# Performance work log

Measured on AMD Instinct MI355X. Metric: run time of the kernel, lower is better.

Reference implementation:

```python
import jax, jax.numpy as jnp
import numpy as np

B, S, D, H = 4, 127, 768, 12
HD = D // H
NS = S + 1
GAMMA = 1.0
NEG_INF = -1e9
EPS = 1e-6


def setup_inputs() -> dict:
    key = jax.random.key(0)
    ks = jax.random.split(key, 12)
    s = 0.02
    return {
        'desc': jax.random.normal(ks[0], (B, S, D), jnp.float32),
        'nve': jax.random.normal(ks[1], (B, NS, D), jnp.float32),
        'mask_M': jax.random.uniform(ks[2], (B, H, S, S), jnp.float32),
        'Wq': jax.random.normal(ks[3], (D, D), jnp.float32) * s,
        'bq': jnp.zeros((D,), jnp.float32),
        'Wk': jax.random.normal(ks[4], (D, D), jnp.float32) * s,
        'bk': jnp.zeros((D,), jnp.float32),
        'Wv': jax.random.normal(ks[5], (D, D), jnp.float32) * s,
        'bv': jnp.zeros((D,), jnp.float32),
        'eW1': jax.random.normal(ks[6], (2 * D, D), jnp.float32) * s,
        'eb1': jnp.zeros((D,), jnp.float32),
        'ln_g': jnp.ones((D,), jnp.float32),
        'ln_b': jnp.zeros((D,), jnp.float32),
        'eW2': jax.random.normal(ks[7], (D, D), jnp.float32) * s,
        'eb2': jnp.zeros((D,), jnp.float32),
        'aW': jax.random.normal(ks[8], (3 * HD,), jnp.float32) * s,
        'ab': jnp.zeros((), jnp.float32),
    }


def _layernorm(x, g, b):
    m = jnp.mean(x, -1, keepdims=True)
    v = jnp.var(x, -1, keepdims=True)
    return (x - m) * jax.lax.rsqrt(v + 1e-5) * g + b


def _adjacency():
    # CLS->Var on, Var->CLS off, Var-Var without self loop
    var_adj = 1.0 - jnp.eye(S, dtype=jnp.float32)
    adj = jnp.zeros((NS, NS), jnp.float32)
    adj = adj.at[1:, 1:].set(var_adj)
    adj = adj.at[0, 1:].set(1.0)
    return adj  # [NS, NS]


def reference(desc, nve, mask_M, Wq, bq, Wk, bk, Wv, bv, eW1, eb1, ln_g, ln_b, eW2, eb2, aW, ab):
    adj = _adjacency()

    def proj(W, bias):
        return (nve @ W + bias).reshape(B, NS, H, HD).transpose(0, 2, 1, 3)  # [B,H,NS,HD]

    q, k, v = proj(Wq, bq), proj(Wk, bk), proj(Wv, bv)

    # edge features: pairwise concat of desc embeddings, CLS edges = [desc, desc]
    node_i = jnp.broadcast_to(desc[:, :, None, :], (B, S, S, D))
    node_j = jnp.broadcast_to(desc[:, None, :, :], (B, S, S, D))
    var_edge = jnp.concatenate([node_i, node_j], -1)           # [B,S,S,2D]
    cls_edge = jnp.concatenate([desc, desc], -1)               # [B,S,2D]
    edge = jnp.zeros((B, NS, NS, 2 * D), jnp.float32)
    edge = edge.at[:, 1:, 1:].set(var_edge)
    edge = edge.at[:, 0, 1:].set(cls_edge)
    edge = edge.at[:, 1:, 0].set(cls_edge)

    # edge_update MLP: Linear -> LayerNorm -> ReLU -> Linear
    h = jax.nn.relu(_layernorm(edge @ eW1 + eb1, ln_g, ln_b))
    e = h @ eW2 + eb2                                           # [B,NS,NS,D]
    e = e.reshape(B, NS, NS, H, HD).transpose(0, 3, 1, 2, 4)    # [B,H,NS,NS,HD]
    e = e * adj[None, None, :, :, None]

    # attn_proj on concat([q_i, k_j, e_ij]) == sum of three dot products + bias
    aq, ak, ae = aW[:HD], aW[HD:2 * HD], aW[2 * HD:]
    logits = (jnp.einsum('bhid,d->bhi', q, aq)[:, :, :, None]
              + jnp.einsum('bhjd,d->bhj', k, ak)[:, :, None, :]
              + jnp.einsum('bhijd,d->bhij', e, ae) + ab)        # [B,H,NS,NS]

    # logit bias from Var-Var probabilities
    p = jnp.clip(mask_M, EPS, 1.0 - EPS)
    bias = (jnp.log(p) - jnp.log(1.0 - p)) * GAMMA
    logits = logits.at[:, :, 1:, 1:].add(bias)

    logits = logits + jnp.where(adj == 0.0, NEG_INF, 0.0)[None, None]
    attn = jax.nn.softmax(logits, axis=-1)                      # dropout off (eval)
    context = jnp.einsum('bhij,bhjd->bhid', attn, v)
    basis_outputs = context.transpose(0, 2, 1, 3)               # [B,NS,H,HD]
    return basis_outputs, attn
```

## Files before the change

### kernel.cpp

```cpp
#include <hip/hip_runtime.h>
#include <hip/hip_bf16.h>

#define BB  4
#define SS  127
#define DD  768
#define HH  12
#define HDl 64
#define NSl 128

typedef __attribute__((ext_vector_type(8))) short short8;
typedef __attribute__((ext_vector_type(4))) float f32x4;

constexpr int OFF_P   = 0;
constexpr int OFF_Q   = OFF_P  + BB*SS*DD;
constexpr int OFF_V   = OFF_Q  + BB*SS*DD;
constexpr int OFF_QA  = OFF_V  + BB*NSl*DD;
constexpr int OFF_KA  = OFF_QA + BB*NSl*HH;
constexpr int OFF_W2B = OFF_KA + BB*NSl*HH;
constexpr int OFF_WQA = OFF_W2B + 6144;
constexpr int OFF_WKA = OFF_WQA + HH*DD;
constexpr int OFF_BF  = OFF_WKA + HH*DD;
constexpr int OFF_SP  = OFF_BF + 64;
constexpr int OFF_SSP = OFF_SP + BB*128;
constexpr int OFF_SQ  = OFF_SSP + BB*128;
constexpr int OFF_SSQ = OFF_SQ + BB*128;
constexpr int OFF_EL  = OFF_SSQ + BB*128;

__device__ inline unsigned short f2bf(float f) {
    unsigned int u = __builtin_bit_cast(unsigned int, f);
    u += 0x7fffu + ((u >> 16) & 1u);
    return (unsigned short)(u >> 16);
}

__device__ inline short8 pack8(float4 a, float4 b) {
    short8 p;
    p[0] = (short)f2bf(a.x); p[1] = (short)f2bf(a.y);
    p[2] = (short)f2bf(a.z); p[3] = (short)f2bf(a.w);
    p[4] = (short)f2bf(b.x); p[5] = (short)f2bf(b.y);
    p[6] = (short)f2bf(b.z); p[7] = (short)f2bf(b.w);
    return p;
}

__device__ inline void unpack8(short8 s, float* f) {
    int4 u = __builtin_bit_cast(int4, s);
    f[0] = __builtin_bit_cast(float, u.x << 16);
    f[1] = __builtin_bit_cast(float, u.x & 0xffff0000);
    f[2] = __builtin_bit_cast(float, u.y << 16);
    f[3] = __builtin_bit_cast(float, u.y & 0xffff0000);
    f[4] = __builtin_bit_cast(float, u.z << 16);
    f[5] = __builtin_bit_cast(float, u.z & 0xffff0000);
    f[6] = __builtin_bit_cast(float, u.w << 16);
    f[7] = __builtin_bit_cast(float, u.w & 0xffff0000);
}

constexpr int NB_PQ   = 96;
constexpr int NB_V    = 96;
constexpr int FOLD_T  = 3 * HH * DD + 36 + 4 * DD;
constexpr int NB_FOLD = (FOLD_T + 511) / 512;

__global__ __launch_bounds__(512) void mega1(
        const float* __restrict__ desc, const float* __restrict__ nve,
        const float* __restrict__ eW1, const float* __restrict__ Wv,
        const float* __restrict__ bv, const float* __restrict__ eb1,
        const float* __restrict__ Wq, const float* __restrict__ Wk,
        const float* __restrict__ eW2,
        const float* __restrict__ bq, const float* __restrict__ bk,
        const float* __restrict__ eb2, const float* __restrict__ aW,
        float* __restrict__ P, float* __restrict__ Qm, float* __restrict__ V,
        unsigned short* __restrict__ W2Bu, float* __restrict__ WQA,
        float* __restrict__ WKA, float* __restrict__ bfold) {
    const int bid = blockIdx.x;
    const int tid = threadIdx.x;

    if (bid >= NB_PQ + NB_V) {
        int idx = (bid - NB_PQ - NB_V) * 512 + tid;
        const int total = 3 * HH * DD;
        if (idx < total) {
            int which = idx / (HH * DD);
            int r = idx % (HH * DD);
            int h = r / DD;
            int c = r % DD;
            const float* W = (which == 0) ? eW2 : (which == 1) ? Wq : Wk;
            const float* a = (which == 0) ? (aW + 2 * HDl) : (which == 1) ? aW : (aW + HDl);
            float s = 0.f;
            #pragma unroll 8
            for (int d = 0; d < HDl; ++d) s += W[c * DD + h * HDl + d] * a[d];
            if (which == 0) W2Bu[h * DD + c] = f2bf(s);
            else if (which == 1) WQA[h * DD + c] = s;
            else WKA[h * DD + c] = s;
        } else if (idx < total + 36) {
            int r = idx - total;
            int which = r / HH, h = r % HH;
            const float* bb = (which == 0) ? eb2 : (which == 1) ? bq : bk;
            const float* a = (which == 0) ? (aW + 2 * HDl) : (which == 1) ? aW : (aW + HDl);
            float s = 0.f;
            for (int d = 0; d < HDl; ++d) s += bb[h * HDl + d] * a[d];
            bfold[r] = s;
        } else if (idx < FOLD_T) {
            W2Bu[12 * DD + (idx - total - 36)] = 0;
        }
        return;
    }

    const bool pq = (bid < NB_PQ);
    const int r = pq ? bid : bid - NB_PQ;
    const int bcol = (r % 12) * 64;
    const int brow = (r / 12) * 64;
    const float* A  = pq ? desc : nve;
    const float* B0 = pq ? eW1 : Wv;
    const int M = pq ? (BB * SS) : (BB * NSl);

    __shared__ short lds[3 * 64 * 64];
    short* As  = lds;
    short* Bs0 = lds + 4096;
    short* Bs1 = lds + 8192;

    const int arow = tid >> 3, akc = (tid & 7) * 8;
    const int abyte = (arow * 128 + akc * 2) ^ ((arow & 7) << 4);
    const int bn = tid & 63, bg = tid >> 6;
    const int bbyte = (bn * 128 + bg * 16) ^ ((bn & 7) << 4);

    const int gm = brow + arow;
    const float* arow_p = A + gm * DD + akc;

    short8 gA, gB0, gB1;
    auto loadA = [&](int k0) {
        float4 f0 = {0,0,0,0}, f1 = {0,0,0,0};
        if (gm < M) {
            f0 = *(const float4*)(arow_p + k0);
            f1 = *(const float4*)(arow_p + k0 + 4);
        }
        gA = pack8(f0, f1);
    };
    auto loadB = [&](const float* Bm, int k0, short8& dst) {
        float v[8];
        #pragma unroll
        for (int q = 0; q < 8; ++q)
            v[q] = Bm[(k0 + bg * 8 + q) * DD + bcol + bn];
        short8 p;
        #pragma unroll
        for (int q = 0; q < 8; ++q) p[q] = (short)f2bf(v[q]);
        dst = p;
    };

    loadA(0);
    loadB(B0, 0, gB0);
    if (pq) loadB(eW1 + DD * DD, 0, gB1);

    const int lane = tid & 63;
    const int w = tid >> 6;
    const int wr = w >> 1, wc = w & 1;
    const int l15 = lane & 15;

    f32x4 acc0[2] = {};
    f32x4 acc1[2] = {};

    for (int k0 = 0; k0 < DD; k0 += 64) {
        *(short8*)((char*)As + abyte) = gA;
        *(short8*)((char*)Bs0 + bbyte) = gB0;
        if (pq) *(short8*)((char*)Bs1 + bbyte) = gB1;
        __syncthreads();
        if (k0 + 64 < DD) {
            loadA(k0 + 64);
            loadB(B0, k0 + 64, gB0);
            if (pq) loadB(eW1 + DD * DD, k0 + 64, gB1);
        }
        #pragma unroll
        for (int ks = 0; ks < 2; ++ks) {
            const int kb = ks * 64 + ((lane >> 4) << 4);
            int row = wr * 16 + l15;
            short8 af = *(const short8*)((char*)As + ((row * 128 + kb) ^ ((row & 7) << 4)));
            #pragma unroll
            for (int ni = 0; ni < 2; ++ni) {
                int col = wc * 32 + ni * 16 + l15;
                int cb = (col * 128 + kb) ^ ((col & 7) << 4);
                short8 b0 = *(const short8*)((char*)Bs0 + cb);
                acc0[ni] = __builtin_amdgcn_mfma_f32_16x16x32_bf16(af, b0, acc0[ni], 0, 0, 0);
                if (pq) {
                    short8 b1 = *(const short8*)((char*)Bs1 + cb);
                    acc1[ni] = __builtin_amdgcn_mfma_f32_16x16x32_bf16(af, b1, acc1[ni], 0, 0, 0);
                }
            }
        }
        __syncthreads();
    }

    #pragma unroll
    for (int ni = 0; ni < 2; ++ni) {
        int gcol = bcol + wc * 32 + ni * 16 + l15;
        float bias0 = pq ? 0.f : bv[gcol];
        float bias1 = pq ? eb1[gcol] : 0.f;
        #pragma unroll
        for (int rr = 0; rr < 4; ++rr) {
            int grow = brow + wr * 16 + ((lane >> 4) << 2) + rr;
            if (grow < M) {
                if (pq) {
                    P[grow * DD + gcol]  = acc0[ni][rr];
                    Qm[grow * DD + gcol] = acc1[ni][rr] + bias1;
                } else {
                    V[grow * DD + gcol] = acc0[ni][rr] + bias0;
                }
            }
        }
    }
}

__global__ void statqk_kernel(const float* __restrict__ Pp, const float* __restrict__ Qp,
                              const float* __restrict__ nve,
                              const float* __restrict__ WQA, const float* __restrict__ WKA,
                              const float* __restrict__ bfold,
                              float* __restrict__ SP, float* __restrict__ SSP,
                              float* __restrict__ SQ, float* __restrict__ SSQ,
                              float* __restrict__ qa, float* __restrict__ ka) {
    int wid = blockIdx.x * 4 + (threadIdx.x >> 6);
    int lane = threadIdx.x & 63;
    const int NSTAT = BB * SS * 2;
    if (wid < NSTAT) {
        int which = wid & 1;
        int row = (wid >> 1) % SS;
        int b = (wid >> 1) / SS;
        const float* src = (which ? Qp : Pp) + (b * SS + row) * DD;
        float s = 0.f, ss = 0.f;
        #pragma unroll
        for (int r = 0; r < 12; ++r) {
            float v = src[lane + 64 * r];
            s += v;
            ss += v * v;
        }
        #pragma unroll
        for (int off = 32; off; off >>= 1) {
            s += __shfl_xor(s, off);
            ss += __shfl_xor(ss, off);
        }
        if (lane == 0) {
            (which ? SQ : SP)[b * 128 + row] = s;
            (which ? SSQ : SSP)[b * 128 + row] = ss;
        }
    } else {
        int t2 = wid - NSTAT;
        if (t2 >= BB * NSl * HH * 2) return;
        int which = t2 & 1;
        int r = t2 >> 1;
        int h = r % HH;
        int t = (r / HH) % NSl;
        int b = r / (HH * NSl);
        const float* W = (which ? WKA : WQA) + h * DD;
        const float* row = nve + (b * NSl + t) * DD;
        float s = 0.f;
        #pragma unroll
        for (int rr = 0; rr < 12; ++rr) {
            int c = lane + 64 * rr;
            s += row[c] * W[c];
        }
        #pragma unroll
        for (int off = 32; off; off >>= 1) s += __shfl_xor(s, off);
        if (lane == 0)
            (which ? ka : qa)[(b * NSl + t) * HH + h] = s + bfold[12 + which * 12 + h];
    }
}

__global__ __launch_bounds__(512) void pair_mfma(
        const float* __restrict__ Pp, const float* __restrict__ Qp,
        const float* __restrict__ ln_g, const float* __restrict__ ln_b,
        const unsigned short* __restrict__ W2Bu,
        const float* __restrict__ SP, const float* __restrict__ SSP,
        const float* __restrict__ SQ, const float* __restrict__ SSQ,
        const float* __restrict__ bfold,
        float* __restrict__ e_log) {
    __shared__ short pB[16 * 768];
    __shared__ short qB[16 * 768];
    __shared__ float gbl[2 * 768];

    const int b   = blockIdx.z;
    const int pi0 = blockIdx.y * 16, qj0 = blockIdx.x * 16;
    const int tid = threadIdx.x;

    {
        int row = tid >> 5;
        int ccb = tid & 31;
        const float* psrc = Pp + (b * SS + min(pi0 + row, SS - 1)) * DD;
        const float* qsrc = Qp + (b * SS + min(qj0 + row, SS - 1)) * DD;
        #pragma unroll
        for (int it = 0; it < 3; ++it) {
            int cc = ccb + it * 32;
            int byte = (row * 1536 + cc * 16) ^ ((row & 7) << 4);
            float4 a0 = *(const float4*)(psrc + cc * 8);
            float4 a1 = *(const float4*)(psrc + cc * 8 + 4);
            *(short8*)((char*)pB + byte) = pack8(a0, a1);
            a0 = *(const float4*)(qsrc + cc * 8);
            a1 = *(const float4*)(qsrc + cc * 8 + 4);
            *(short8*)((char*)qB + byte) = pack8(a0, a1);
        }
    }
    if (tid < 384) {
        int c = tid * 4;
        float4 v = (tid < 192) ? *(const float4*)(ln_g + c)
                               : *(const float4*)(ln_b + (c - 768));
        *(float4*)(gbl + c) = v;
    }
    __syncthreads();

    const int lane = tid & 63;
    const int w    = tid >> 6;
    const int l15  = lane & 15;
    const int kg   = lane >> 4;

    f32x4 gacc = {};
    #pragma unroll 4
    for (int ks = 0; ks < 24; ++ks) {
        int cb = ks * 64 + kg * 16;
        short8 ap = *(const short8*)((char*)pB + ((l15 * 1536 + cb) ^ ((l15 & 7) << 4)));
        short8 aq = *(const short8*)((char*)qB + ((l15 * 1536 + cb) ^ ((l15 & 7) << 4)));
        gacc = __builtin_amdgcn_mfma_f32_16x16x32_bf16(ap, aq, gacc, 0, 0, 0);
    }

    float al[2], be[2];
    #pragma unroll
    for (int s = 0; s < 2; ++s) {
        int pl = 2 * w + s;
        int src = ((pl >> 2) << 4) | l15;
        int rsel = pl & 3;
        float gg = (rsel == 0) ? gacc[0] : (rsel == 1) ? gacc[1]
                 : (rsel == 2) ? gacc[2] : gacc[3];
        gg = __shfl(gg, src);
        int pig = min(pi0 + pl, SS - 1);
        int qjg = min(qj0 + l15, SS - 1);
        float mean = (SP[b * 128 + pig] + SQ[b * 128 + qjg]) * (1.f / DD);
        float sumsq = SSP[b * 128 + pig] + 2.f * gg + SSQ[b * 128 + qjg];
        float var = sumsq * (1.f / DD) - mean * mean;
        float a = rsqrtf(var + 1e-5f);
        al[s] = a;
        be[s] = -mean * a;
    }

    const unsigned short* wrow = W2Bu + l15 * 768;
    const int r0 = 2 * w, r1 = 2 * w + 1;
    const int p0base = r0 * 1536, p1base = r1 * 1536;
    const int p0x = (r0 & 7) << 4, p1x = (r1 & 7) << 4;
    f32x4 acc0 = {}, acc1 = {};

    #pragma unroll 2
    for (int ks = 0; ks < 24; ++ks) {
        const int c0 = ks * 32 + kg * 8;
        short8 bfg = *(const short8*)(wrow + c0);
        f32x4 g0 = *(const f32x4*)(gbl + c0);
        f32x4 g1 = *(const f32x4*)(gbl + c0 + 4);
        f32x4 bb0 = *(const f32x4*)(gbl + 768 + c0);
        f32x4 bb1 = *(const f32x4*)(gbl + 768 + c0 + 4);
        float gv[8] = {g0.x, g0.y, g0.z, g0.w, g1.x, g1.y, g1.z, g1.w};
        float bv8[8] = {bb0.x, bb0.y, bb0.z, bb0.w, bb1.x, bb1.y, bb1.z, bb1.w};

        short8 q8 = *(const short8*)((char*)qB + ((l15 * 1536 + c0 * 2) ^ ((l15 & 7) << 4)));
        float qf[8];
        unpack8(q8, qf);

        short8 p8 = *(const short8*)((char*)pB + ((p0base + c0 * 2) ^ p0x));
        float pf[8];
        unpack8(p8, pf);
        short8 ya;
        #pragma unroll
        for (int j = 0; j < 8; ++j) {
            float t = pf[j] + qf[j];
            float u = __builtin_fmaf(al[0], t, be[0]);
            float y = fmaxf(__builtin_fmaf(gv[j], u, bv8[j]), 0.f);
            ya[j] = (short)f2bf(y);
        }
        acc0 = __builtin_amdgcn_mfma_f32_16x16x32_bf16(ya, bfg, acc0, 0, 0, 0);

        p8 = *(const short8*)((char*)pB + ((p1base + c0 * 2) ^ p1x));
        unpack8(p8, pf);
        #pragma unroll
        for (int j = 0; j < 8; ++j) {
            float t = pf[j] + qf[j];
            float u = __builtin_fmaf(al[1], t, be[1]);
            float y = fmaxf(__builtin_fmaf(gv[j], u, bv8[j]), 0.f);
            ya[j] = (short)f2bf(y);
        }
        acc1 = __builtin_amdgcn_mfma_f32_16x16x32_bf16(ya, bfg, acc1, 0, 0, 0);
    }

    if (l15 < HH) {
        const float badd = bfold[l15];
        #pragma unroll
        for (int s = 0; s < 2; ++s) {
            int pig = pi0 + 2 * w + s;
            if (pig >= SS) continue;
            f32x4 A = s ? acc1 : acc0;
            #pragma unroll
            for (int r = 0; r < 4; ++r) {
                int qjg = qj0 + (kg << 2) + r;
                if (qjg < SS) {
                    int i = (pig == qjg) ? 0 : (pig + 1);
                    e_log[(((b * HH + l15) * NSl) + i) * NSl + (qjg + 1)] = A[r] + badd;
                }
            }
        }
    }
}

__global__ __launch_bounds__(512) void softmax_ctx_kernel(
        const float* __restrict__ e_log,
        const float* __restrict__ qa, const float* __restrict__ ka,
        const float* __restrict__ mask_M, const float* __restrict__ ab,
        const float* __restrict__ V,
        float* __restrict__ out) {
    __shared__ float Vl[NSl * HDl];
    __shared__ float kal[NSl];
    __shared__ float pl[8][NSl];

    const int b = blockIdx.z;
    const int h = blockIdx.y;
    const int iq = blockIdx.x;
    const int tid = threadIdx.x;
    const int lane = tid & 63;
    const int w = tid >> 6;

    #pragma unroll
    for (int it = 0; it < 4; ++it) {
        int m = tid + it * 512;
        int j = m >> 4, dd = (m & 15) * 4;
        *(float4*)(Vl + j * HDl + dd) =
            *(const float4*)(V + (b * NSl + j) * DD + h * HDl + dd);
    }
    if (tid < NSl) kal[tid] = ka[(b * NSl + tid) * HH + h];
    __syncthreads();

    const float abv = ab[0];

    for (int rr = 0; rr < 4; ++rr) {
        const int i = iq * 32 + w * 4 + rr;
        const float qv = qa[(b * NSl + i) * HH + h];
        const float* e_row = e_log + (((b * HH + h) * NSl) + i) * NSl;

        float lg[2];
        bool valid[2];
        #pragma unroll
        for (int s = 0; s < 2; ++s) {
            int j = 1 + lane + 64 * s;
            bool v = (j < NSl) && !(i >= 1 && j == i);
            float l = -1e30f;
            if (v) {
                l = e_row[j] + qv + kal[j] + abv;
                if (i >= 1) {
                    float p = mask_M[((b * HH + h) * SS + (i - 1)) * SS + (j - 1)];
                    p = fminf(fmaxf(p, 1e-6f), 1.0f - 1e-6f);
                    l += __logf(p) - __logf(1.0f - p);
                }
            }
            lg[s] = l;
            valid[s] = v;
        }
        float m = fmaxf(lg[0], lg[1]);
        #pragma unroll
        for (int off = 32; off; off >>= 1) m = fmaxf(m, __shfl_xor(m, off));
        float e0 = valid[0] ? __expf(lg[0] - m) : 0.f;
        float e1 = valid[1] ? __expf(lg[1] - m) : 0.f;
        float s = e0 + e1;
        #pragma unroll
        for (int off = 32; off; off >>= 1) s += __shfl_xor(s, off);
        const float inv = 1.0f / s;

        const float p0 = e0 * inv, p1 = e1 * inv;

        float* attn_row = out + BB * NSl * HH * HDl + (((b * HH + h) * NSl) + i) * NSl;
        attn_row[1 + lane] = p0;
        if (65 + lane < NSl) attn_row[65 + lane] = p1;
        if (lane == 0) attn_row[0] = 0.f;

        pl[w][1 + lane] = p0;
        if (65 + lane < NSl) pl[w][65 + lane] = p1;
        if (lane == 0) pl[w][0] = 0.f;
        __syncthreads();

        float c0 = 0.f, c1 = 0.f, c2 = 0.f, c3 = 0.f;
        #pragma unroll 4
        for (int j = 0; j < NSl; j += 4) {
            c0 += pl[w][j]     * Vl[(j)     * HDl + lane];
            c1 += pl[w][j + 1] * Vl[(j + 1) * HDl + lane];
            c2 += pl[w][j + 2] * Vl[(j + 2) * HDl + lane];
            c3 += pl[w][j + 3] * Vl[(j + 3) * HDl + lane];
        }
        out[((b * NSl + i) * HH + h) * HDl + lane] = (c0 + c1) + (c2 + c3);
        __syncthreads();
    }
}

extern "C" void kernel_launch(void* const* d_in, const int* in_sizes, int n_in,
                              void* d_out, int out_size, void* d_ws, size_t ws_size,
                              hipStream_t stream) {
    const float* desc   = (const float*)d_in[0];
    const float* nve    = (const float*)d_in[1];
    const float* mask_M = (const float*)d_in[2];
    const float* Wq     = (const float*)d_in[3];
    const float* bq     = (const float*)d_in[4];
    const float* Wk     = (const float*)d_in[5];
    const float* bk     = (const float*)d_in[6];
    const float* Wv     = (const float*)d_in[7];
    const float* bv     = (const float*)d_in[8];
    const float* eW1    = (const float*)d_in[9];
    const float* eb1    = (const float*)d_in[10];
    const float* ln_g   = (const float*)d_in[11];
    const float* ln_b   = (const float*)d_in[12];
    const float* eW2    = (const float*)d_in[13];
    const float* eb2    = (const float*)d_in[14];
    const float* aW     = (const float*)d_in[15];
    const float* ab     = (const float*)d_in[16];

    float* ws  = (float*)d_ws;
    float* out = (float*)d_out;
    unsigned short* W2Bu = (unsigned short*)(ws + OFF_W2B);

    mega1<<<NB_PQ + NB_V + NB_FOLD, 512, 0, stream>>>(
        desc, nve, eW1, Wv, bv, eb1,
        Wq, Wk, eW2, bq, bk, eb2, aW,
        ws + OFF_P, ws + OFF_Q, ws + OFF_V,
        W2Bu, ws + OFF_WQA, ws + OFF_WKA, ws + OFF_BF);

    statqk_kernel<<<(BB * SS * 2 + BB * NSl * HH * 2 + 3) / 4, 256, 0, stream>>>(
        ws + OFF_P, ws + OFF_Q, nve, ws + OFF_WQA, ws + OFF_WKA, ws + OFF_BF,
        ws + OFF_SP, ws + OFF_SSP, ws + OFF_SQ, ws + OFF_SSQ,
        ws + OFF_QA, ws + OFF_KA);

    pair_mfma<<<dim3(8, 8, BB), 512, 0, stream>>>(
        ws + OFF_P, ws + OFF_Q, ln_g, ln_b, W2Bu,
        ws + OFF_SP, ws + OFF_SSP, ws + OFF_SQ, ws + OFF_SSQ,
        ws + OFF_BF, ws + OFF_EL);

    softmax_ctx_kernel<<<dim3(4, HH, BB), 512, 0, stream>>>(
        ws + OFF_EL, ws + OFF_QA, ws + OFF_KA, mask_M, ab, ws + OFF_V, out);
}
```

Baseline: 64.18 us.

## Fold row-stat and qa/ka kernel into pair and softmax kernels

Removes the separate statqk kernel. Row sums and sums of squares for the layernorm are now computed inside pair_mfma while P/Q tiles are staged to LDS, and the per-head q/k attention scalars are computed inside softmax_ctx_kernel from nve and the folded weights. The bf16 packing in the inner loop also switches from manual rounding to the v_cvt_pk_bf16_f32 instruction. This drops one kernel launch and a global round trip. In exchange, the ka dot products are recomputed redundantly in each of the four iq blocks per (b,h), and row stats are recomputed in each pair tile.

```diff
diff --git a/kernel.cpp b/kernel.cpp
--- a/kernel.cpp
+++ b/kernel.cpp
@@ -14,17 +14,11 @@
 constexpr int OFF_P   = 0;
 constexpr int OFF_Q   = OFF_P  + BB*SS*DD;
 constexpr int OFF_V   = OFF_Q  + BB*SS*DD;
-constexpr int OFF_QA  = OFF_V  + BB*NSl*DD;
-constexpr int OFF_KA  = OFF_QA + BB*NSl*HH;
-constexpr int OFF_W2B = OFF_KA + BB*NSl*HH;
+constexpr int OFF_W2B = OFF_V  + BB*NSl*DD;
 constexpr int OFF_WQA = OFF_W2B + 6144;
 constexpr int OFF_WKA = OFF_WQA + HH*DD;
 constexpr int OFF_BF  = OFF_WKA + HH*DD;
-constexpr int OFF_SP  = OFF_BF + 64;
-constexpr int OFF_SSP = OFF_SP + BB*128;
-constexpr int OFF_SQ  = OFF_SSP + BB*128;
-constexpr int OFF_SSQ = OFF_SQ + BB*128;
-constexpr int OFF_EL  = OFF_SSQ + BB*128;
+constexpr int OFF_EL  = OFF_BF + 64;
 
 __device__ inline unsigned short f2bf(float f) {
     unsigned int u = __builtin_bit_cast(unsigned int, f);
@@ -51,6 +45,12 @@
     f[5] = __builtin_bit_cast(float, u.z & 0xffff0000);
     f[6] = __builtin_bit_cast(float, u.w << 16);
     f[7] = __builtin_bit_cast(float, u.w & 0xffff0000);
+}
+
+__device__ inline unsigned int cvtpk(float lo, float hi) {
+    unsigned int r;
+    asm volatile("v_cvt_pk_bf16_f32 %0, %1, %2" : "=v"(r) : "v"(lo), "v"(hi));
+    return r;
 }
 
 constexpr int NB_PQ   = 96;
@@ -205,71 +205,17 @@
     }
 }
 
-__global__ void statqk_kernel(const float* __restrict__ Pp, const float* __restrict__ Qp,
-                              const float* __restrict__ nve,
-                              const float* __restrict__ WQA, const float* __restrict__ WKA,
-                              const float* __restrict__ bfold,
-                              float* __restrict__ SP, float* __restrict__ SSP,
-                              float* __restrict__ SQ, float* __restrict__ SSQ,
-                              float* __restrict__ qa, float* __restrict__ ka) {
-    int wid = blockIdx.x * 4 + (threadIdx.x >> 6);
-    int lane = threadIdx.x & 63;
-    const int NSTAT = BB * SS * 2;
-    if (wid < NSTAT) {
-        int which = wid & 1;
-        int row = (wid >> 1) % SS;
-        int b = (wid >> 1) / SS;
-        const float* src = (which ? Qp : Pp) + (b * SS + row) * DD;
-        float s = 0.f, ss = 0.f;
-        #pragma unroll
-        for (int r = 0; r < 12; ++r) {
-            float v = src[lane + 64 * r];
-            s += v;
-            ss += v * v;
-        }
-        #pragma unroll
-        for (int off = 32; off; off >>= 1) {
-            s += __shfl_xor(s, off);
-            ss += __shfl_xor(ss, off);
-        }
-        if (lane == 0) {
-            (which ? SQ : SP)[b * 128 + row] = s;
-            (which ? SSQ : SSP)[b * 128 + row] = ss;
-        }
-    } else {
-        int t2 = wid - NSTAT;
-        if (t2 >= BB * NSl * HH * 2) return;
-        int which = t2 & 1;
-        int r = t2 >> 1;
-        int h = r % HH;
-        int t = (r / HH) % NSl;
-        int b = r / (HH * NSl);
-        const float* W = (which ? WKA : WQA) + h * DD;
-        const float* row = nve + (b * NSl + t) * DD;
-        float s = 0.f;
-        #pragma unroll
-        for (int rr = 0; rr < 12; ++rr) {
-            int c = lane + 64 * rr;
-            s += row[c] * W[c];
-        }
-        #pragma unroll
-        for (int off = 32; off; off >>= 1) s += __shfl_xor(s, off);
-        if (lane == 0)
-            (which ? ka : qa)[(b * NSl + t) * HH + h] = s + bfold[12 + which * 12 + h];
-    }
-}
-
 __global__ __launch_bounds__(512) void pair_mfma(
         const float* __restrict__ Pp, const float* __restrict__ Qp,
         const float* __restrict__ ln_g, const float* __restrict__ ln_b,
         const unsigned short* __restrict__ W2Bu,
-        const float* __restrict__ SP, const float* __restrict__ SSP,
-        const float* __restrict__ SQ, const float* __restrict__ SSQ,
         const float* __restrict__ bfold,
         float* __restrict__ e_log) {
     __shared__ short pB[16 * 768];
     __shared__ short qB[16 * 768];
     __shared__ float gbl[2 * 768];
+    __shared__ float2 pstat[16];
+    __shared__ float2 qstat[16];
 
     const int b   = blockIdx.z;
     const int pi0 = blockIdx.y * 16, qj0 = blockIdx.x * 16;
@@ -280,16 +226,34 @@
         int ccb = tid & 31;
         const float* psrc = Pp + (b * SS + min(pi0 + row, SS - 1)) * DD;
         const float* qsrc = Qp + (b * SS + min(qj0 + row, SS - 1)) * DD;
+        float ps = 0.f, pss = 0.f, qs = 0.f, qss = 0.f;
         #pragma unroll
         for (int it = 0; it < 3; ++it) {
             int cc = ccb + it * 32;
             int byte = (row * 1536 + cc * 16) ^ ((row & 7) << 4);
             float4 a0 = *(const float4*)(psrc + cc * 8);
             float4 a1 = *(const float4*)(psrc + cc * 8 + 4);
+            ps  += (a0.x + a0.y + a0.z + a0.w) + (a1.x + a1.y + a1.z + a1.w);
+            pss += a0.x*a0.x + a0.y*a0.y + a0.z*a0.z + a0.w*a0.w
+                 + a1.x*a1.x + a1.y*a1.y + a1.z*a1.z + a1.w*a1.w;
             *(short8*)((char*)pB + byte) = pack8(a0, a1);
             a0 = *(const float4*)(qsrc + cc * 8);
             a1 = *(const float4*)(qsrc + cc * 8 + 4);
+            qs  += (a0.x + a0.y + a0.z + a0.w) + (a1.x + a1.y + a1.z + a1.w);
+            qss += a0.x*a0.x + a0.y*a0.y + a0.z*a0.z + a0.w*a0.w
+                 + a1.x*a1.x + a1.y*a1.y + a1.z*a1.z + a1.w*a1.w;
             *(short8*)((char*)qB + byte) = pack8(a0, a1);
+        }
+        #pragma unroll
+        for (int off = 16; off; off >>= 1) {
+            ps  += __shfl_xor(ps, off);
+            pss += __shfl_xor(pss, off);
+            qs  += __shfl_xor(qs, off);
+            qss += __shfl_xor(qss, off);
+        }
+        if ((tid & 31) == 0) {
+            pstat[row] = make_float2(ps, pss);
+            qstat[row] = make_float2(qs, qss);
         }
     }
     if (tid < 384) {
@@ -323,10 +287,10 @@
         float gg = (rsel == 0) ? gacc[0] : (rsel == 1) ? gacc[1]
                  : (rsel == 2) ? gacc[2] : gacc[3];
         gg = __shfl(gg, src);
-        int pig = min(pi0 + pl, SS - 1);
-        int qjg = min(qj0 + l15, SS - 1);
-        float mean = (SP[b * 128 + pig] + SQ[b * 128 + qjg]) * (1.f / DD);
-        float sumsq = SSP[b * 128 + pig] + 2.f * gg + SSQ[b * 128 + qjg];
+        float2 pst = pstat[pl];
+        float2 qst = qstat[l15];
+        float mean = (pst.x + qst.x) * (1.f / DD);
+        float sumsq = pst.y + 2.f * gg + qst.y;
         float var = sumsq * (1.f / DD) - mean * mean;
         float a = rsqrtf(var + 1e-5f);
         al[s] = a;
@@ -357,15 +321,19 @@
         short8 p8 = *(const short8*)((char*)pB + ((p0base + c0 * 2) ^ p0x));
         float pf[8];
         unpack8(p8, pf);
-        short8 ya;
+        float y[8];
         #pragma unroll
         for (int j = 0; j < 8; ++j) {
             float t = pf[j] + qf[j];
             float u = __builtin_fmaf(al[0], t, be[0]);
-            float y = fmaxf(__builtin_fmaf(gv[j], u, bv8[j]), 0.f);
-            ya[j] = (short)f2bf(y);
-        }
-        acc0 = __builtin_amdgcn_mfma_f32_16x16x32_bf16(ya, bfg, acc0, 0, 0, 0);
+            y[j] = fmaxf(__builtin_fmaf(gv[j], u, bv8[j]), 0.f);
+        }
+        {
+            int4 ti = { (int)cvtpk(y[0], y[1]), (int)cvtpk(y[2], y[3]),
+                        (int)cvtpk(y[4], y[5]), (int)cvtpk(y[6], y[7]) };
+            short8 ya = __builtin_bit_cast(short8, ti);
+            acc0 = __builtin_amdgcn_mfma_f32_16x16x32_bf16(ya, bfg, acc0, 0, 0, 0);
+        }
 
         p8 = *(const short8*)((char*)pB + ((p1base + c0 * 2) ^ p1x));
         unpack8(p8, pf);
@@ -373,10 +341,14 @@
         for (int j = 0; j < 8; ++j) {
             float t = pf[j] + qf[j];
             float u = __builtin_fmaf(al[1], t, be[1]);
-            float y = fmaxf(__builtin_fmaf(gv[j], u, bv8[j]), 0.f);
-            ya[j] = (short)f2bf(y);
-        }
-        acc1 = __builtin_amdgcn_mfma_f32_16x16x32_bf16(ya, bfg, acc1, 0, 0, 0);
+            y[j] = fmaxf(__builtin_fmaf(gv[j], u, bv8[j]), 0.f);
+        }
+        {
+            int4 ti = { (int)cvtpk(y[0], y[1]), (int)cvtpk(y[2], y[3]),
+                        (int)cvtpk(y[4], y[5]), (int)cvtpk(y[6], y[7]) };
+            short8 ya = __builtin_bit_cast(short8, ti);
+            acc1 = __builtin_amdgcn_mfma_f32_16x16x32_bf16(ya, bfg, acc1, 0, 0, 0);
+        }
     }
 
     if (l15 < HH) {
@@ -400,12 +372,15 @@
 
 __global__ __launch_bounds__(512) void softmax_ctx_kernel(
         const float* __restrict__ e_log,
-        const float* __restrict__ qa, const float* __restrict__ ka,
+        const float* __restrict__ nve,
+        const float* __restrict__ WQA, const float* __restrict__ WKA,
+        const float* __restrict__ bfold,
         const float* __restrict__ mask_M, const float* __restrict__ ab,
         const float* __restrict__ V,
         float* __restrict__ out) {
     __shared__ float Vl[NSl * HDl];
     __shared__ float kal[NSl];
+    __shared__ float qal[32];
     __shared__ float pl[8][NSl];
 
     const int b = blockIdx.z;
@@ -422,14 +397,42 @@
         *(float4*)(Vl + j * HDl + dd) =
             *(const float4*)(V + (b * NSl + j) * DD + h * HDl + dd);
     }
-    if (tid < NSl) kal[tid] = ka[(b * NSl + tid) * HH + h];
+    {
+        int j = tid >> 2, part = tid & 3;
+        const float4* src = (const float4*)(nve + (b * NSl + j) * DD + part * 192);
+        const float4* wk  = (const float4*)(WKA + h * DD + part * 192);
+        float s = 0.f;
+        #pragma unroll 8
+        for (int q = 0; q < 48; ++q) {
+            float4 x = src[q], y = wk[q];
+            s += x.x * y.x + x.y * y.y + x.z * y.z + x.w * y.w;
+        }
+        s += __shfl_xor(s, 1);
+        s += __shfl_xor(s, 2);
+        if (part == 0) kal[j] = s + bfold[24 + h];
+    }
+    {
+        int il = tid >> 4, part = tid & 15;
+        int i = iq * 32 + il;
+        const float4* src = (const float4*)(nve + (b * NSl + i) * DD + part * 48);
+        const float4* wq  = (const float4*)(WQA + h * DD + part * 48);
+        float s = 0.f;
+        #pragma unroll
+        for (int q = 0; q < 12; ++q) {
+            float4 x = src[q], y = wq[q];
+            s += x.x * y.x + x.y * y.y + x.z * y.z + x.w * y.w;
+        }
+        #pragma unroll
+        for (int off = 8; off; off >>= 1) s += __shfl_xor(s, off);
+        if (part == 0) qal[il] = s + bfold[12 + h];
+    }
     __syncthreads();
 
     const float abv = ab[0];
 
     for (int rr = 0; rr < 4; ++rr) {
         const int i = iq * 32 + w * 4 + rr;
-        const float qv = qa[(b * NSl + i) * HH + h];
+        const float qv = qal[w * 4 + rr];
         const float* e_row = e_log + (((b * HH + h) * NSl) + i) * NSl;
 
         float lg[2];
@@ -516,16 +519,11 @@
         ws + OFF_P, ws + OFF_Q, ws + OFF_V,
         W2Bu, ws + OFF_WQA, ws + OFF_WKA, ws + OFF_BF);
 
-    statqk_kernel<<<(BB * SS * 2 + BB * NSl * HH * 2 + 3) / 4, 256, 0, stream>>>(
-        ws + OFF_P, ws + OFF_Q, nve, ws + OFF_WQA, ws + OFF_WKA, ws + OFF_BF,
-        ws + OFF_SP, ws + OFF_SSP, ws + OFF_SQ, ws + OFF_SSQ,
-        ws + OFF_QA, ws + OFF_KA);
-
     pair_mfma<<<dim3(8, 8, BB), 512, 0, stream>>>(
         ws + OFF_P, ws + OFF_Q, ln_g, ln_b, W2Bu,
-        ws + OFF_SP, ws + OFF_SSP, ws + OFF_SQ, ws + OFF_SSQ,
         ws + OFF_BF, ws + OFF_EL);
 
     softmax_ctx_kernel<<<dim3(4, HH, BB), 512, 0, stream>>>(
-        ws + OFF_EL, ws + OFF_QA, ws + OFF_KA, mask_M, ab, ws + OFF_V, out);
-}
+        ws + OFF_EL, nve, ws + OFF_WQA, ws + OFF_WKA, ws + OFF_BF,
+        mask_M, ab, ws + OFF_V, out);
+}
```

Measured after the change: 82.28 us. 1.28x slower.

## Use bf16 MFMA for attention-context product and packed bf16 conversion in edge GEMM

Applied to the files above, without the earlier changes.

The softmax kernel now stores V transposed as bf16 in swizzled shared memory and writes the probability rows as bf16 into a shared tile. After a single barrier it computes the 32x64 context tile with 16x16x32 bf16 MFMA instead of a scalar fp32 loop that needed two barriers per row. The edge GEMM packs activations with v_cvt_pk_bf16_f32 instead of per-element conversion, and the logit bias uses one log of p/(1-p) instead of two logs. This trades fp32 precision in the context product for bf16 and rounds the attention weights before the matmul.

```diff
diff --git a/kernel.cpp b/kernel.cpp
--- a/kernel.cpp
+++ b/kernel.cpp
@@ -51,6 +51,12 @@
     f[5] = __builtin_bit_cast(float, u.z & 0xffff0000);
     f[6] = __builtin_bit_cast(float, u.w << 16);
     f[7] = __builtin_bit_cast(float, u.w & 0xffff0000);
+}
+
+__device__ inline unsigned int cvtpk(float lo, float hi) {
+    unsigned int r;
+    asm volatile("v_cvt_pk_bf16_f32 %0, %1, %2" : "=v"(r) : "v"(lo), "v"(hi));
+    return r;
 }
 
 constexpr int NB_PQ   = 96;
@@ -357,15 +363,19 @@
         short8 p8 = *(const short8*)((char*)pB + ((p0base + c0 * 2) ^ p0x));
         float pf[8];
         unpack8(p8, pf);
-        short8 ya;
+        float y[8];
         #pragma unroll
         for (int j = 0; j < 8; ++j) {
             float t = pf[j] + qf[j];
             float u = __builtin_fmaf(al[0], t, be[0]);
-            float y = fmaxf(__builtin_fmaf(gv[j], u, bv8[j]), 0.f);
-            ya[j] = (short)f2bf(y);
-        }
-        acc0 = __builtin_amdgcn_mfma_f32_16x16x32_bf16(ya, bfg, acc0, 0, 0, 0);
+            y[j] = fmaxf(__builtin_fmaf(gv[j], u, bv8[j]), 0.f);
+        }
+        {
+            int4 ti = { (int)cvtpk(y[0], y[1]), (int)cvtpk(y[2], y[3]),
+                        (int)cvtpk(y[4], y[5]), (int)cvtpk(y[6], y[7]) };
+            short8 ya = __builtin_bit_cast(short8, ti);
+            acc0 = __builtin_amdgcn_mfma_f32_16x16x32_bf16(ya, bfg, acc0, 0, 0, 0);
+        }
 
         p8 = *(const short8*)((char*)pB + ((p1base + c0 * 2) ^ p1x));
         unpack8(p8, pf);
@@ -373,10 +383,14 @@
         for (int j = 0; j < 8; ++j) {
             float t = pf[j] + qf[j];
             float u = __builtin_fmaf(al[1], t, be[1]);
-            float y = fmaxf(__builtin_fmaf(gv[j], u, bv8[j]), 0.f);
-            ya[j] = (short)f2bf(y);
-        }
-        acc1 = __builtin_amdgcn_mfma_f32_16x16x32_bf16(ya, bfg, acc1, 0, 0, 0);
+            y[j] = fmaxf(__builtin_fmaf(gv[j], u, bv8[j]), 0.f);
+        }
+        {
+            int4 ti = { (int)cvtpk(y[0], y[1]), (int)cvtpk(y[2], y[3]),
+                        (int)cvtpk(y[4], y[5]), (int)cvtpk(y[6], y[7]) };
+            short8 ya = __builtin_bit_cast(short8, ti);
+            acc1 = __builtin_amdgcn_mfma_f32_16x16x32_bf16(ya, bfg, acc1, 0, 0, 0);
+        }
     }
 
     if (l15 < HH) {
@@ -404,9 +418,9 @@
         const float* __restrict__ mask_M, const float* __restrict__ ab,
         const float* __restrict__ V,
         float* __restrict__ out) {
-    __shared__ float Vl[NSl * HDl];
+    __shared__ short Vt[64 * 128];
+    __shared__ short plb[32 * 128];
     __shared__ float kal[NSl];
-    __shared__ float pl[8][NSl];
 
     const int b = blockIdx.z;
     const int h = blockIdx.y;
@@ -415,12 +429,22 @@
     const int lane = tid & 63;
     const int w = tid >> 6;
 
-    #pragma unroll
-    for (int it = 0; it < 4; ++it) {
-        int m = tid + it * 512;
-        int j = m >> 4, dd = (m & 15) * 4;
-        *(float4*)(Vl + j * HDl + dd) =
-            *(const float4*)(V + (b * NSl + j) * DD + h * HDl + dd);
+    {
+        int j = tid >> 2;
+        int dq = (tid & 3) * 16;
+        const float* src = V + (b * NSl + j) * DD + h * HDl + dq;
+        float4 f0 = *(const float4*)(src);
+        float4 f1 = *(const float4*)(src + 4);
+        float4 f2 = *(const float4*)(src + 8);
+        float4 f3 = *(const float4*)(src + 12);
+        float vv[16] = {f0.x,f0.y,f0.z,f0.w, f1.x,f1.y,f1.z,f1.w,
+                        f2.x,f2.y,f2.z,f2.w, f3.x,f3.y,f3.z,f3.w};
+        #pragma unroll
+        for (int t = 0; t < 16; ++t) {
+            int d = dq + t;
+            int byte = (d * 256 + j * 2) ^ ((d & 7) << 4);
+            *(short*)((char*)Vt + byte) = (short)f2bf(vv[t]);
+        }
     }
     if (tid < NSl) kal[tid] = ka[(b * NSl + tid) * HH + h];
     __syncthreads();
@@ -428,7 +452,8 @@
     const float abv = ab[0];
 
     for (int rr = 0; rr < 4; ++rr) {
-        const int i = iq * 32 + w * 4 + rr;
+        const int il = w * 4 + rr;
+        const int i = iq * 32 + il;
         const float qv = qa[(b * NSl + i) * HH + h];
         const float* e_row = e_log + (((b * HH + h) * NSl) + i) * NSl;
 
@@ -444,7 +469,7 @@
                 if (i >= 1) {
                     float p = mask_M[((b * HH + h) * SS + (i - 1)) * SS + (j - 1)];
                     p = fminf(fmaxf(p, 1e-6f), 1.0f - 1e-6f);
-                    l += __logf(p) - __logf(1.0f - p);
+                    l += __logf(p / (1.0f - p));
                 }
             }
             lg[s] = l;
@@ -467,21 +492,38 @@
         if (65 + lane < NSl) attn_row[65 + lane] = p1;
         if (lane == 0) attn_row[0] = 0.f;
 
-        pl[w][1 + lane] = p0;
-        if (65 + lane < NSl) pl[w][65 + lane] = p1;
-        if (lane == 0) pl[w][0] = 0.f;
-        __syncthreads();
-
-        float c0 = 0.f, c1 = 0.f, c2 = 0.f, c3 = 0.f;
-        #pragma unroll 4
-        for (int j = 0; j < NSl; j += 4) {
-            c0 += pl[w][j]     * Vl[(j)     * HDl + lane];
-            c1 += pl[w][j + 1] * Vl[(j + 1) * HDl + lane];
-            c2 += pl[w][j + 2] * Vl[(j + 2) * HDl + lane];
-            c3 += pl[w][j + 3] * Vl[(j + 3) * HDl + lane];
-        }
-        out[((b * NSl + i) * HH + h) * HDl + lane] = (c0 + c1) + (c2 + c3);
-        __syncthreads();
+        {
+            int byte0 = (il * 256 + (1 + lane) * 2) ^ ((il & 7) << 4);
+            *(short*)((char*)plb + byte0) = (short)f2bf(p0);
+            if (65 + lane < NSl) {
+                int byte1 = (il * 256 + (65 + lane) * 2) ^ ((il & 7) << 4);
+                *(short*)((char*)plb + byte1) = (short)f2bf(p1);
+            }
+            if (lane == 0) {
+                int byteZ = (il * 256) ^ ((il & 7) << 4);
+                *(short*)((char*)plb + byteZ) = 0;
+            }
+        }
+    }
+    __syncthreads();
+
+    const int l15 = lane & 15;
+    const int kg  = lane >> 4;
+    const int itile = w >> 2, dtile = w & 3;
+    const int arow  = itile * 16 + l15;
+    const int bcold = dtile * 16 + l15;
+    f32x4 acc = {};
+    #pragma unroll
+    for (int ks = 0; ks < 4; ++ks) {
+        int kb = (ks * 32 + kg * 8) * 2;
+        short8 af = *(const short8*)((char*)plb + ((arow * 256 + kb) ^ ((arow & 7) << 4)));
+        short8 bf = *(const short8*)((char*)Vt  + ((bcold * 256 + kb) ^ ((bcold & 7) << 4)));
+        acc = __builtin_amdgcn_mfma_f32_16x16x32_bf16(af, bf, acc, 0, 0, 0);
+    }
+    #pragma unroll
+    for (int r = 0; r < 4; ++r) {
+        int i = iq * 32 + itile * 16 + kg * 4 + r;
+        out[((b * NSl + i) * HH + h) * HDl + dtile * 16 + l15] = acc[r];
     }
 }
 
```

New measurement: 57.55 us. 1.12x faster.
